# Optimization experiments

Measured on AMD Instinct MI355X. Metric: run time of the kernel, lower is better.

## Reference

```python
import jax, jax.numpy as jnp
import numpy as np

NUM_EMB = 4096
EMB_DIM = 256
COMMIT = 0.25


def setup_inputs() -> dict:
    key = jax.random.key(0)
    k1, k2 = jax.random.split(key)
    z = jax.random.normal(k1, (64, 32, 32, EMB_DIM), dtype=jnp.float32)
    # torch init: uniform(-1/K, 1/K)
    codebook = jax.random.uniform(k2, (NUM_EMB, EMB_DIM), dtype=jnp.float32,
                                  minval=-1.0 / NUM_EMB, maxval=1.0 / NUM_EMB)
    return {"z": z, "codebook": codebook}


def reference(z, codebook):
    zf = z.reshape(-1, EMB_DIM)                       # [N, D]
    # ||z||^2 - 2 z.e + ||e||^2  -> [N, K]
    d = (jnp.sum(zf * zf, axis=1, keepdims=True)
         - 2.0 * (zf @ codebook.T)
         + jnp.sum(codebook * codebook, axis=1))
    idx = jnp.argmin(d, axis=1)                       # [N]
    z_q = codebook[idx].reshape(z.shape)              # gather replaces one-hot matmul
    sg = jax.lax.stop_gradient
    loss = jnp.mean((sg(z_q) - z) ** 2) + COMMIT * jnp.mean((z_q - sg(z)) ** 2)
    z_q_ste = z + sg(z_q - z)                         # straight-through
    return z_q_ste, loss
```

## Files before the change

### kernel.cpp

```cpp
#include <hip/hip_runtime.h>
#include <hip/hip_bf16.h>
#include <stdint.h>

#define NUM_EMB 4096
#define EMB_DIM 256
#define NVEC 65536
#define OUT0_SIZE (NVEC * EMB_DIM)
#define MTILE 128
#define NTILE 64
#define LROW 528
#define DCONST 0.0625f

typedef __bf16 bf16x8 __attribute__((ext_vector_type(8)));
typedef float floatx16 __attribute__((ext_vector_type(16)));

static __device__ __forceinline__ unsigned int f2bf(float f) {
  unsigned int u = __float_as_uint(f);
  return (u + 0x7fffu + ((u >> 16) & 1u)) >> 16;
}

static __device__ __forceinline__ uint4 pack_bf8(float4 a, float4 b) {
  uint4 r;
  r.x = f2bf(a.x) | (f2bf(a.y) << 16);
  r.y = f2bf(a.z) | (f2bf(a.w) << 16);
  r.z = f2bf(b.x) | (f2bf(b.y) << 16);
  r.w = f2bf(b.z) | (f2bf(b.w) << 16);
  return r;
}

__global__ void __launch_bounds__(256) vq_prep(const float* __restrict__ cbf,
                                               unsigned short* __restrict__ cbb,
                                               float* __restrict__ enorm,
                                               float* __restrict__ out) {
  int w = threadIdx.x >> 6;
  int lane = threadIdx.x & 63;
  int row = blockIdx.x * 4 + w;
  float4 v = ((const float4*)(cbf + (size_t)row * EMB_DIM))[lane];
  float ss = v.x * v.x + v.y * v.y + v.z * v.z + v.w * v.w;
  ushort4 b;
  b.x = (unsigned short)f2bf(v.x);
  b.y = (unsigned short)f2bf(v.y);
  b.z = (unsigned short)f2bf(v.z);
  b.w = (unsigned short)f2bf(v.w);
  ((ushort4*)(cbb + (size_t)row * EMB_DIM))[lane] = b;
#pragma unroll
  for (int m = 1; m < 64; m <<= 1) ss += __shfl_xor(ss, m, 64);
  if (lane == 0) enorm[row] = ss + DCONST;
  if (blockIdx.x == 0 && threadIdx.x == 0) out[OUT0_SIZE] = 0.0f;
}

__global__ void __launch_bounds__(256, 2) vq_main(const float* __restrict__ z,
                                                  const float* __restrict__ cbf,
                                                  const unsigned short* __restrict__ cbb,
                                                  const float* __restrict__ enorm,
                                                  float* __restrict__ out) {
  __shared__ unsigned char stage[NTILE * LROW];
  __shared__ float lds_en[NTILE];
  __shared__ unsigned int minlds[2][MTILE];
  __shared__ float znorm[MTILE];
  __shared__ int idx_lds[MTILE];
  __shared__ float wsum[4];

  const int t = threadIdx.x;
  const int w = t >> 6;
  const int lane = t & 63;
  const int h = lane >> 5;
  const int eL = lane & 31;
  const int rg = w & 1;
  const int cg = w >> 1;
  const int blk = blockIdx.x;
  const int row_base = blk * MTILE + rg * 64;

  uint4 afrag[2][16];
  float zn[2] = {0.f, 0.f};
#pragma unroll
  for (int g = 0; g < 2; ++g) {
    const float* rp = z + (size_t)(row_base + g * 32 + eL) * EMB_DIM + h * 8;
#pragma unroll
    for (int ks = 0; ks < 16; ++ks) {
      float4 a0 = *(const float4*)(rp + ks * 16);
      float4 a1 = *(const float4*)(rp + ks * 16 + 4);
      zn[g] += a0.x * a0.x + a0.y * a0.y + a0.z * a0.z + a0.w * a0.w
             + a1.x * a1.x + a1.y * a1.y + a1.z * a1.z + a1.w * a1.w;
      afrag[g][ks] = pack_bf8(a0, a1);
    }
    zn[g] += __shfl_xor(zn[g], 32, 64);
  }
  if (w < 2 && h == 0) {
    znorm[rg * 64 + eL] = zn[0];
    znorm[rg * 64 + 32 + eL] = zn[1];
  }

  unsigned int pmin[32];
#pragma unroll
  for (int s = 0; s < 32; ++s) pmin[s] = 0xFFFFFFFFu;

  for (int c0 = 0; c0 < NUM_EMB; c0 += NTILE) {
    __syncthreads();
#pragma unroll
    for (int j = 0; j < 8; ++j) {
      int id = t + 256 * j;
      int e = id >> 5, kc = id & 31;
      uint4 v = *(const uint4*)(cbb + (size_t)(c0 + e) * EMB_DIM + kc * 8);
      *(uint4*)(stage + e * LROW + kc * 16) = v;
    }
    if (t < NTILE) lds_en[t] = enorm[c0 + t];
    __syncthreads();

    floatx16 acc0, acc1;
#pragma unroll
    for (int r = 0; r < 16; ++r) { acc0[r] = 0.f; acc1[r] = 0.f; }
    const unsigned char* bp = stage + (cg * 32 + eL) * LROW + h * 16;
#pragma unroll
    for (int ks = 0; ks < 16; ++ks) {
      bf16x8 b = __builtin_bit_cast(bf16x8, *(const uint4*)(bp + ks * 32));
      acc0 = __builtin_amdgcn_mfma_f32_32x32x16_bf16(
          __builtin_bit_cast(bf16x8, afrag[0][ks]), b, acc0, 0, 0, 0);
      acc1 = __builtin_amdgcn_mfma_f32_32x32x16_bf16(
          __builtin_bit_cast(bf16x8, afrag[1][ks]), b, acc1, 0, 0, 0);
    }

    float enC = lds_en[cg * 32 + eL];
    unsigned int colb = (unsigned int)(c0 + cg * 32 + eL);
#pragma unroll
    for (int reg = 0; reg < 16; ++reg) {
      float d0 = fmaf(-2.f, acc0[reg], enC);
      unsigned int p0 = (__float_as_uint(d0) & 0xFFFFF000u) | colb;
      if (p0 < pmin[reg]) pmin[reg] = p0;
      float d1 = fmaf(-2.f, acc1[reg], enC);
      unsigned int p1 = (__float_as_uint(d1) & 0xFFFFF000u) | colb;
      if (p1 < pmin[16 + reg]) pmin[16 + reg] = p1;
    }
  }

#pragma unroll
  for (int s = 0; s < 32; ++s) {
    unsigned int v = pmin[s];
#pragma unroll
    for (int m = 1; m <= 16; m <<= 1) {
      unsigned int o = __shfl_xor(v, m, 64);
      if (o < v) v = o;
    }
    pmin[s] = v;
  }
  if (eL == 0) {
#pragma unroll
    for (int s = 0; s < 32; ++s) {
      int g = s >> 4, reg = s & 15;
      int rowl = rg * 64 + g * 32 + (reg & 3) + 8 * (reg >> 2) + 4 * h;
      minlds[cg][rowl] = pmin[s];
    }
  }
  __syncthreads();

  float rl = 0.f;
  if (t < MTILE) {
    unsigned int m0 = minlds[0][t], m1 = minlds[1][t];
    unsigned int m = m1 < m0 ? m1 : m0;
    idx_lds[t] = (int)(m & 0xFFFu);
    rl = znorm[t] + __uint_as_float(m & 0xFFFFF000u) - DCONST;
  }
#pragma unroll
  for (int m = 1; m < 64; m <<= 1) rl += __shfl_xor(rl, m, 64);
  if (lane == 0) wsum[w] = rl;
  __syncthreads();
  if (t == 0) {
    float s = (wsum[0] + wsum[1]) + (wsum[2] + wsum[3]);
    atomicAdd(out + OUT0_SIZE, s * (1.25f / (float)OUT0_SIZE));
  }

#pragma unroll 4
  for (int j = 0; j < 32; ++j) {
    int id4 = j * 256 + t;
    int r = id4 >> 6, c4 = id4 & 63;
    int k = idx_lds[r];
    float4 ev = ((const float4*)(cbf + (size_t)k * EMB_DIM))[c4];
    ((float4*)(out + (size_t)(blk * MTILE + r) * EMB_DIM))[c4] = ev;
  }
}

extern "C" void kernel_launch(void* const* d_in, const int* in_sizes, int n_in,
                              void* d_out, int out_size, void* d_ws, size_t ws_size,
                              hipStream_t stream) {
  const float* z = (const float*)d_in[0];
  const float* cbf = (const float*)d_in[1];
  unsigned short* cbb = (unsigned short*)d_ws;
  float* enorm = (float*)((char*)d_ws + (size_t)NUM_EMB * EMB_DIM * 2);
  float* out = (float*)d_out;
  vq_prep<<<NUM_EMB / 4, 256, 0, stream>>>(cbf, cbb, enorm, out);
  vq_main<<<NVEC / MTILE, 256, 0, stream>>>(z, cbf, cbb, enorm, out);
}
```

Baseline: 260.5 us.

## Stream codebook fragments from global into registers with double buffering, drop LDS staging

Replaces the LDS-staged codebook tiles and per-tile __syncthreads with direct per-wave global/L2 loads of bf16 codebook fragments into registers. The loads are double-buffered so the next 32-entry tile is fetched while the current one is computed. The MFMA shape also changes from 32x32x16 to 16x16x32 with four row groups. This removes the barriers and LDS traffic, but every wave now reads the codebook from L2 itself with no sharing through LDS, which raises cache bandwidth demand and register pressure.

```diff
diff --git a/kernel.cpp b/kernel.cpp
--- a/kernel.cpp
+++ b/kernel.cpp
@@ -7,12 +7,11 @@
 #define NVEC 65536
 #define OUT0_SIZE (NVEC * EMB_DIM)
 #define MTILE 128
-#define NTILE 64
-#define LROW 528
+#define NTILE 32
 #define DCONST 0.0625f
 
 typedef __bf16 bf16x8 __attribute__((ext_vector_type(8)));
-typedef float floatx16 __attribute__((ext_vector_type(16)));
+typedef float floatx4 __attribute__((ext_vector_type(4)));
 
 static __device__ __forceinline__ unsigned int f2bf(float f) {
   unsigned int u = __float_as_uint(f);
@@ -54,8 +53,6 @@
                                                   const unsigned short* __restrict__ cbb,
                                                   const float* __restrict__ enorm,
                                                   float* __restrict__ out) {
-  __shared__ unsigned char stage[NTILE * LROW];
-  __shared__ float lds_en[NTILE];
   __shared__ unsigned int minlds[2][MTILE];
   __shared__ float znorm[MTILE];
   __shared__ int idx_lds[MTILE];
@@ -64,92 +61,103 @@
   const int t = threadIdx.x;
   const int w = t >> 6;
   const int lane = t & 63;
-  const int h = lane >> 5;
-  const int eL = lane & 31;
+  const int q = lane >> 4;
+  const int i = lane & 15;
   const int rg = w & 1;
   const int cg = w >> 1;
   const int blk = blockIdx.x;
   const int row_base = blk * MTILE + rg * 64;
 
-  uint4 afrag[2][16];
-  float zn[2] = {0.f, 0.f};
-#pragma unroll
-  for (int g = 0; g < 2; ++g) {
-    const float* rp = z + (size_t)(row_base + g * 32 + eL) * EMB_DIM + h * 8;
-#pragma unroll
-    for (int ks = 0; ks < 16; ++ks) {
-      float4 a0 = *(const float4*)(rp + ks * 16);
-      float4 a1 = *(const float4*)(rp + ks * 16 + 4);
-      zn[g] += a0.x * a0.x + a0.y * a0.y + a0.z * a0.z + a0.w * a0.w
-             + a1.x * a1.x + a1.y * a1.y + a1.z * a1.z + a1.w * a1.w;
+  uint4 afrag[4][8];
+  float zn[4];
+#pragma unroll
+  for (int g = 0; g < 4; ++g) {
+    const float* rp = z + (size_t)(row_base + g * 16 + i) * EMB_DIM + q * 8;
+    float s = 0.f;
+#pragma unroll
+    for (int ks = 0; ks < 8; ++ks) {
+      float4 a0 = *(const float4*)(rp + ks * 32);
+      float4 a1 = *(const float4*)(rp + ks * 32 + 4);
+      s += a0.x * a0.x + a0.y * a0.y + a0.z * a0.z + a0.w * a0.w
+         + a1.x * a1.x + a1.y * a1.y + a1.z * a1.z + a1.w * a1.w;
       afrag[g][ks] = pack_bf8(a0, a1);
     }
-    zn[g] += __shfl_xor(zn[g], 32, 64);
-  }
-  if (w < 2 && h == 0) {
-    znorm[rg * 64 + eL] = zn[0];
-    znorm[rg * 64 + 32 + eL] = zn[1];
-  }
-
-  unsigned int pmin[32];
-#pragma unroll
-  for (int s = 0; s < 32; ++s) pmin[s] = 0xFFFFFFFFu;
-
-  for (int c0 = 0; c0 < NUM_EMB; c0 += NTILE) {
-    __syncthreads();
-#pragma unroll
-    for (int j = 0; j < 8; ++j) {
-      int id = t + 256 * j;
-      int e = id >> 5, kc = id & 31;
-      uint4 v = *(const uint4*)(cbb + (size_t)(c0 + e) * EMB_DIM + kc * 8);
-      *(uint4*)(stage + e * LROW + kc * 16) = v;
-    }
-    if (t < NTILE) lds_en[t] = enorm[c0 + t];
-    __syncthreads();
-
-    floatx16 acc0, acc1;
-#pragma unroll
-    for (int r = 0; r < 16; ++r) { acc0[r] = 0.f; acc1[r] = 0.f; }
-    const unsigned char* bp = stage + (cg * 32 + eL) * LROW + h * 16;
-#pragma unroll
-    for (int ks = 0; ks < 16; ++ks) {
-      bf16x8 b = __builtin_bit_cast(bf16x8, *(const uint4*)(bp + ks * 32));
-      acc0 = __builtin_amdgcn_mfma_f32_32x32x16_bf16(
-          __builtin_bit_cast(bf16x8, afrag[0][ks]), b, acc0, 0, 0, 0);
-      acc1 = __builtin_amdgcn_mfma_f32_32x32x16_bf16(
-          __builtin_bit_cast(bf16x8, afrag[1][ks]), b, acc1, 0, 0, 0);
-    }
-
-    float enC = lds_en[cg * 32 + eL];
-    unsigned int colb = (unsigned int)(c0 + cg * 32 + eL);
-#pragma unroll
-    for (int reg = 0; reg < 16; ++reg) {
-      float d0 = fmaf(-2.f, acc0[reg], enC);
-      unsigned int p0 = (__float_as_uint(d0) & 0xFFFFF000u) | colb;
-      if (p0 < pmin[reg]) pmin[reg] = p0;
-      float d1 = fmaf(-2.f, acc1[reg], enC);
-      unsigned int p1 = (__float_as_uint(d1) & 0xFFFFF000u) | colb;
-      if (p1 < pmin[16 + reg]) pmin[16 + reg] = p1;
-    }
-  }
-
-#pragma unroll
-  for (int s = 0; s < 32; ++s) {
+    s += __shfl_xor(s, 16, 64);
+    s += __shfl_xor(s, 32, 64);
+    zn[g] = s;
+  }
+  if (w < 2 && lane < 16) {
+#pragma unroll
+    for (int g = 0; g < 4; ++g) znorm[rg * 64 + g * 16 + i] = zn[g];
+  }
+
+  unsigned int pmin[16];
+#pragma unroll
+  for (int s = 0; s < 16; ++s) pmin[s] = 0xFFFFFFFFu;
+
+  const unsigned short* bp = cbb + ((size_t)(cg * 16 + i) * EMB_DIM + q * 8);
+  const float* ep = enorm + cg * 16 + i;
+
+  uint4 bA[8], bB[8];
+  float enA, enB;
+#pragma unroll
+  for (int ks = 0; ks < 8; ++ks) bA[ks] = *(const uint4*)(bp + ks * 32);
+  enA = ep[0];
+
+#define VQ_COMPUTE(BUF, EN, C0)                                              \
+  {                                                                          \
+    floatx4 acc[4];                                                          \
+    _Pragma("unroll") for (int g = 0; g < 4; ++g) acc[g] = (floatx4){0.f, 0.f, 0.f, 0.f}; \
+    _Pragma("unroll") for (int ks = 0; ks < 8; ++ks) {                       \
+      bf16x8 bb = __builtin_bit_cast(bf16x8, BUF[ks]);                       \
+      _Pragma("unroll") for (int g = 0; g < 4; ++g)                          \
+        acc[g] = __builtin_amdgcn_mfma_f32_16x16x32_bf16(                    \
+            __builtin_bit_cast(bf16x8, afrag[g][ks]), bb, acc[g], 0, 0, 0);  \
+    }                                                                        \
+    unsigned int colb = (unsigned int)((C0) + cg * 16 + i);                  \
+    _Pragma("unroll") for (int g = 0; g < 4; ++g)                            \
+      _Pragma("unroll") for (int r = 0; r < 4; ++r) {                        \
+        float d = fmaf(-2.f, acc[g][r], EN);                                 \
+        unsigned int p = (__float_as_uint(d) & 0xFFFFF000u) | colb;          \
+        unsigned int* pm = &pmin[g * 4 + r];                                 \
+        if (p < *pm) *pm = p;                                                \
+      }                                                                      \
+  }
+
+  for (int tile = 0; tile < NUM_EMB / NTILE; tile += 2) {
+    {
+      const unsigned short* p1 = bp + (size_t)(tile + 1) * NTILE * EMB_DIM;
+#pragma unroll
+      for (int ks = 0; ks < 8; ++ks) bB[ks] = *(const uint4*)(p1 + ks * 32);
+      enB = ep[(tile + 1) * NTILE];
+    }
+    VQ_COMPUTE(bA, enA, tile * NTILE);
+    {
+      int t2 = (tile + 2 < NUM_EMB / NTILE) ? tile + 2 : 0;
+      const unsigned short* p2 = bp + (size_t)t2 * NTILE * EMB_DIM;
+#pragma unroll
+      for (int ks = 0; ks < 8; ++ks) bA[ks] = *(const uint4*)(p2 + ks * 32);
+      enA = ep[t2 * NTILE];
+    }
+    VQ_COMPUTE(bB, enB, (tile + 1) * NTILE);
+  }
+
+#pragma unroll
+  for (int s = 0; s < 16; ++s) {
     unsigned int v = pmin[s];
 #pragma unroll
-    for (int m = 1; m <= 16; m <<= 1) {
+    for (int m = 1; m <= 8; m <<= 1) {
       unsigned int o = __shfl_xor(v, m, 64);
       if (o < v) v = o;
     }
     pmin[s] = v;
   }
-  if (eL == 0) {
-#pragma unroll
-    for (int s = 0; s < 32; ++s) {
-      int g = s >> 4, reg = s & 15;
-      int rowl = rg * 64 + g * 32 + (reg & 3) + 8 * (reg >> 2) + 4 * h;
-      minlds[cg][rowl] = pmin[s];
-    }
+  if (i == 0) {
+#pragma unroll
+    for (int g = 0; g < 4; ++g)
+#pragma unroll
+      for (int r = 0; r < 4; ++r)
+        minlds[cg][rg * 64 + g * 16 + q * 4 + r] = pmin[g * 4 + r];
   }
   __syncthreads();
 
```

New measurement: 363.6 us. +39.6%, slower.
